# Kernel optimization log

Hardware: AMD Instinct MI355X
Metric: run time of the kernel (lower is better)

## Reference

```python
import jax, jax.numpy as jnp
import numpy as np

DIM = 512
N_HEADS = 8
HEAD_DIM = DIM // N_HEADS


def rope_pos(T, head_dim, dtype=jnp.float32):
    inv_freq = 1.0 / (10000.0 ** (jnp.arange(0, head_dim, 2, dtype=jnp.float32) / head_dim))
    t = jnp.arange(T, dtype=jnp.float32)
    freqs = jnp.einsum('i,j->ij', t, inv_freq)            # [T, head_dim/2]
    return jnp.concatenate([freqs, freqs], axis=-1).astype(dtype)  # [T, head_dim]


def rotate_half(x):
    x1, x2 = jnp.split(x, 2, axis=-1)
    return jnp.concatenate([-x2, x1], axis=-1)


def apply_rope(pos, t):
    # pos: [T, hd] -> broadcast to [1,1,T,hd]; t: [B,H,T,hd]
    pos = pos[None, None, :, :]
    return t * jnp.cos(pos) + rotate_half(t) * jnp.sin(pos)


def setup_inputs() -> dict:
    key = jax.random.key(0)
    ks = jax.random.split(key, 6)
    B, T = 4, 2048
    x = jax.random.normal(ks[0], (B, T, DIM), dtype=jnp.float32)
    mask = jnp.zeros((B, T), dtype=jnp.float32)  # additive mask
    s = 1.0 / np.sqrt(DIM)
    qkv_w = jax.random.normal(ks[1], (3 * DIM, DIM), dtype=jnp.float32) * s
    qkv_b = jnp.zeros((3 * DIM,), dtype=jnp.float32)
    proj_w = jax.random.normal(ks[2], (DIM, DIM), dtype=jnp.float32) * s
    proj_b = jnp.zeros((DIM,), dtype=jnp.float32)
    return {"x": x, "mask": mask, "qkv_w": qkv_w, "qkv_b": qkv_b,
            "proj_w": proj_w, "proj_b": proj_b}


def reference(x, mask, qkv_w, qkv_b, proj_w, proj_b):
    B, T, C = x.shape
    qkv = x @ qkv_w.T + qkv_b                       # [B,T,3C]
    qkv = qkv.reshape(B, T, 3, N_HEADS, HEAD_DIM)
    q, k, v = qkv[:, :, 0], qkv[:, :, 1], qkv[:, :, 2]  # [B,T,H,hd]
    q = q.transpose(0, 2, 1, 3)                     # [B,H,T,hd]
    k = k.transpose(0, 2, 1, 3)
    v = v.transpose(0, 2, 1, 3)
    pos = rope_pos(T, HEAD_DIM, x.dtype)
    q = apply_rope(pos, q)
    k = apply_rope(pos, k)
    scores = jnp.einsum('bhqd,bhkd->bhqk', q, k) * (1.0 / np.sqrt(HEAD_DIM))
    scores = scores + mask[:, None, None, :]        # 2D mask -> [B,1,1,T]
    probs = jax.nn.softmax(scores.astype(jnp.float32), axis=-1).astype(x.dtype)
    # dropout is identity in eval mode
    out = jnp.einsum('bhqk,bhkd->bhqd', probs, v)   # [B,H,T,hd]
    out = out.transpose(0, 2, 1, 3).reshape(B, T, C)
    return out @ proj_w.T + proj_b
```

## Files before the change

kernel.cpp:

```cpp
#include <hip/hip_runtime.h>
#include <math.h>


typedef __attribute__((ext_vector_type(8))) short bf16x8;
typedef __attribute__((ext_vector_type(4))) float floatx4;

#define LOG2E 1.44269504088896f

__device__ __forceinline__ unsigned short f2bf(float f) {
  unsigned int u = __float_as_uint(f);
  u += 0x7fffu + ((u >> 16) & 1u);
  return (unsigned short)(u >> 16);
}

__device__ __forceinline__ unsigned int cvtpk_bf16(float a, float b) {
  unsigned int r;
  asm("v_cvt_pk_bf16_f32 %0, %1, %2" : "=v"(r) : "v"(a), "v"(b));
  return r;
}

__device__ __forceinline__ void gld_lds16(unsigned short* lds, const unsigned short* g) {
  __builtin_amdgcn_global_load_lds(
      (const __attribute__((address_space(1))) unsigned int*)g,
      (__attribute__((address_space(3))) unsigned int*)lds, 16, 0, 0);
}

__global__ __launch_bounds__(256) void prep_kernel(
    const float* __restrict__ x, const float* __restrict__ wq, const float* __restrict__ wp,
    unsigned short* __restrict__ xb, unsigned short* __restrict__ wqb,
    unsigned short* __restrict__ wpb, float* __restrict__ cosT, float* __restrict__ sinT) {
  int i = blockIdx.x * 256 + threadIdx.x;
  if (i < 655360) {
    int base = i * 8;
    const float* src;
    unsigned short* dst;
    int j;
    if (base < 4194304)      { src = x;  dst = xb;  j = base; }
    else if (base < 4980736) { src = wq; dst = wqb; j = base - 4194304; }
    else                     { src = wp; dst = wpb; j = base - 4980736; }
    float4 a = *(const float4*)(src + j);
    float4 b = *(const float4*)(src + j + 4);
    uint4 r;
    r.x = cvtpk_bf16(a.x, a.y);
    r.y = cvtpk_bf16(a.z, a.w);
    r.z = cvtpk_bf16(b.x, b.y);
    r.w = cvtpk_bf16(b.z, b.w);
    *(uint4*)(dst + j) = r;
  } else if (i < 720896) {
    int j = i - 655360;
    int t = j >> 5, f = j & 31;
    double fr = (double)t * pow(10000.0, -(double)f / 32.0);
    cosT[j] = (float)cos(fr);
    sinT[j] = (float)sin(fr);
  }
}

__global__ __launch_bounds__(256) void qkv_kernel(
    const unsigned short* __restrict__ xb, const unsigned short* __restrict__ wqb,
    const float* __restrict__ qkv_b, const float* __restrict__ cosT,
    const float* __restrict__ sinT, unsigned short* __restrict__ Qb,
    unsigned short* __restrict__ Kb, unsigned short* __restrict__ Vtb) {
  __shared__ __align__(16) unsigned short SM[2][2][128 * 32];
  const int tid = threadIdx.x;
  const int wave = tid >> 6, lane = tid & 63, ln = lane & 15, quad = lane >> 4;
  const int m0 = blockIdx.x * 128, n0 = blockIdx.y * 128;
  const int wr = (wave >> 1) * 64, wc = (wave & 1) * 64;

  floatx4 acc[4][4];
#pragma unroll
  for (int i = 0; i < 4; ++i)
#pragma unroll
    for (int j = 0; j < 4; ++j) acc[i][j] = (floatx4){0.f, 0.f, 0.f, 0.f};

  const int c0 = tid, c1 = tid + 256;
  const int ar0 = c0 >> 2, ak0 = (c0 & 3) * 8;
  const int ar1 = c1 >> 2, ak1 = (c1 & 3) * 8;

  gld_lds16(SM[0][0] + c0 * 8, xb + (size_t)(m0 + ar0) * 512 + ak0);
  gld_lds16(SM[0][0] + c1 * 8, xb + (size_t)(m0 + ar1) * 512 + ak1);
  gld_lds16(SM[0][1] + c0 * 8, wqb + (size_t)(n0 + ar0) * 512 + ak0);
  gld_lds16(SM[0][1] + c1 * 8, wqb + (size_t)(n0 + ar1) * 512 + ak1);
  __syncthreads();

  for (int kt = 0; kt < 16; ++kt) {
    const int cur = kt & 1;
    if (kt < 15) {
      const int kn = (kt + 1) * 32;
      gld_lds16(SM[cur ^ 1][0] + c0 * 8, xb + (size_t)(m0 + ar0) * 512 + kn + ak0);
      gld_lds16(SM[cur ^ 1][0] + c1 * 8, xb + (size_t)(m0 + ar1) * 512 + kn + ak1);
      gld_lds16(SM[cur ^ 1][1] + c0 * 8, wqb + (size_t)(n0 + ar0) * 512 + kn + ak0);
      gld_lds16(SM[cur ^ 1][1] + c1 * 8, wqb + (size_t)(n0 + ar1) * 512 + kn + ak1);
    }
    bf16x8 af[4], bfb[4];
#pragma unroll
    for (int mi = 0; mi < 4; ++mi)
      af[mi] = *(const bf16x8*)(SM[cur][0] + (wr + mi * 16 + ln) * 32 + quad * 8);
#pragma unroll
    for (int ni = 0; ni < 4; ++ni)
      bfb[ni] = *(const bf16x8*)(SM[cur][1] + (wc + ni * 16 + ln) * 32 + quad * 8);
#pragma unroll
    for (int mi = 0; mi < 4; ++mi)
#pragma unroll
      for (int ni = 0; ni < 4; ++ni)
        acc[mi][ni] = __builtin_amdgcn_mfma_f32_16x16x32_bf16(af[mi], bfb[ni], acc[mi][ni], 0, 0, 0);
    __syncthreads();
  }

  const int colbase = n0 + wc;
  const int mat = colbase >> 9;
  float bias[4];
#pragma unroll
  for (int ni = 0; ni < 4; ++ni) bias[ni] = qkv_b[colbase + ni * 16 + ln];

  if (mat == 2) {
    unsigned short* Ts = &SM[0][0][0];
#pragma unroll
    for (int mi = 0; mi < 4; ++mi) {
      int r0 = wr + mi * 16 + quad * 4;
#pragma unroll
      for (int ni = 0; ni < 4; ++ni) {
        int c = wc + ni * 16 + ln;
        ushort4 pk;
        pk.x = f2bf(acc[mi][ni][0] + bias[ni]);
        pk.y = f2bf(acc[mi][ni][1] + bias[ni]);
        pk.z = f2bf(acc[mi][ni][2] + bias[ni]);
        pk.w = f2bf(acc[mi][ni][3] + bias[ni]);
        *(ushort4*)(Ts + c * 128 + (r0 ^ ((c & 7) << 3))) = pk;
      }
    }
    __syncthreads();
    const int d2 = tid >> 1, seg = tid & 1;
    const int h0 = (n0 & 511) >> 6;
    const int hh = d2 >> 6, dd = d2 & 63;
    const int bidx = m0 >> 11, tl0 = m0 & 2047;
    unsigned short* dst = Vtb + ((size_t)(bidx * 8 + h0 + hh) * 64 + dd) * 2048 + tl0;
    const int xr = (d2 & 7) << 3;
#pragma unroll
    for (int j = 0; j < 8; ++j) {
      int g = seg * 64 + j * 8;
      uint4 v = *(const uint4*)(Ts + d2 * 128 + (g ^ xr));
      *(uint4*)(dst + g) = v;
    }
  } else {
    const int h = (colbase & 511) >> 6;
    unsigned short* dst = (mat == 0) ? Qb : Kb;
    const float sc = (mat == 0) ? 0.125f * LOG2E : 1.0f;
#pragma unroll
    for (int mi = 0; mi < 4; ++mi) {
#pragma unroll
      for (int r = 0; r < 4; ++r) {
        int row = m0 + wr + mi * 16 + quad * 4 + r;
        int bidx = row >> 11, t = row & 2047;
        const float* cr = cosT + t * 32;
        const float* sr = sinT + t * 32;
        size_t obase = ((size_t)(bidx * 8 + h) * 2048 + t) * 64;
#pragma unroll
        for (int ni = 0; ni < 2; ++ni) {
          int dlo = ni * 16 + ln;
          float cv = cr[dlo], sv = sr[dlo];
          float xlo = acc[mi][ni][r] + bias[ni];
          float xhi = acc[mi][ni + 2][r] + bias[ni + 2];
          dst[obase + dlo]      = f2bf((xlo * cv - xhi * sv) * sc);
          dst[obase + dlo + 32] = f2bf((xhi * cv + xlo * sv) * sc);
        }
      }
    }
  }
}

__global__ __launch_bounds__(512) void attn_kernel(
    const unsigned short* __restrict__ Qb, const unsigned short* __restrict__ Kb,
    const unsigned short* __restrict__ Vtb, const float* __restrict__ mask,
    unsigned short* __restrict__ attnb) {
  __shared__ __align__(16) unsigned short Ks[2][64 * 64];
  __shared__ __align__(16) unsigned short Vs[2][64 * 64];
  __shared__ __align__(16) unsigned short Ps[128 * 64];

  const int tid = threadIdx.x;
  const int wave = tid >> 6, lane = tid & 63, ln = lane & 15, quad = lane >> 4;
  const int swz = (ln & 7) << 3;
  const int bh = blockIdx.y;
  const int b = bh >> 3, h = bh & 7;
  const int q0 = blockIdx.x * 128;
  const int wq = wave * 16;

  const unsigned short* Qhead = Qb + (size_t)bh * 2048 * 64;
  const unsigned short* Khead = Kb + (size_t)bh * 2048 * 64;
  const unsigned short* Vhead = Vtb + (size_t)bh * 64 * 2048;

  bf16x8 qf[2];
#pragma unroll
  for (int ks = 0; ks < 2; ++ks)
    qf[ks] = *(const bf16x8*)(Qhead + (size_t)(q0 + wq + ln) * 64 + ks * 32 + quad * 8);

  floatx4 o[4];
#pragma unroll
  for (int mi2 = 0; mi2 < 4; ++mi2) o[mi2] = (floatx4){0.f, 0.f, 0.f, 0.f};
  float mrun = -INFINITY;
  float lrun = 0.f;

  const int srow = tid >> 3;
  const int scol = (tid & 7) * 8;
  const int sdst = srow * 64 + (scol ^ ((srow & 7) << 3));

  {
    uint4 k0v = *(const uint4*)(Khead + (size_t)srow * 64 + scol);
    uint4 v0v = *(const uint4*)(Vhead + (size_t)srow * 2048 + scol);
    *(uint4*)(Ks[0] + sdst) = k0v;
    *(uint4*)(Vs[0] + sdst) = v0v;
  }
  __syncthreads();

  for (int kt = 0; kt < 32; ++kt) {
    const int cur = kt & 1;
    const int k0 = kt * 64;
    uint4 kpre, vpre;
    if (kt < 31) {
      kpre = *(const uint4*)(Khead + (size_t)(k0 + 64 + srow) * 64 + scol);
      vpre = *(const uint4*)(Vhead + (size_t)srow * 2048 + k0 + 64 + scol);
    }

    floatx4 sm[4];
#pragma unroll
    for (int mi = 0; mi < 4; ++mi) {
      bf16x8 kf0 = *(const bf16x8*)(Ks[cur] + (mi * 16 + ln) * 64 + ((quad * 8) ^ swz));
      bf16x8 kf1 = *(const bf16x8*)(Ks[cur] + (mi * 16 + ln) * 64 + ((32 + quad * 8) ^ swz));
      floatx4 a = (floatx4){0.f, 0.f, 0.f, 0.f};
      a = __builtin_amdgcn_mfma_f32_16x16x32_bf16(kf0, qf[0], a, 0, 0, 0);
      a = __builtin_amdgcn_mfma_f32_16x16x32_bf16(kf1, qf[1], a, 0, 0, 0);
      sm[mi] = a;
    }
#pragma unroll
    for (int mi = 0; mi < 4; ++mi) {
      float4 mv = *(const float4*)(mask + b * 2048 + k0 + mi * 16 + quad * 4);
      sm[mi][0] += mv.x * LOG2E; sm[mi][1] += mv.y * LOG2E;
      sm[mi][2] += mv.z * LOG2E; sm[mi][3] += mv.w * LOG2E;
    }
    float vmax = fmaxf(fmaxf(sm[0][0], sm[0][1]), fmaxf(sm[0][2], sm[0][3]));
#pragma unroll
    for (int mi = 1; mi < 4; ++mi)
      vmax = fmaxf(vmax, fmaxf(fmaxf(sm[mi][0], sm[mi][1]), fmaxf(sm[mi][2], sm[mi][3])));
    vmax = fmaxf(vmax, __shfl_xor(vmax, 16));
    vmax = fmaxf(vmax, __shfl_xor(vmax, 32));
    if (__any(vmax > mrun)) {
      float nm = fmaxf(mrun, vmax);
      float alpha = exp2f(mrun - nm);
      mrun = nm;
      lrun *= alpha;
#pragma unroll
      for (int mi2 = 0; mi2 < 4; ++mi2) {
        o[mi2][0] *= alpha; o[mi2][1] *= alpha;
        o[mi2][2] *= alpha; o[mi2][3] *= alpha;
      }
    }
    float psum = 0.f;
#pragma unroll
    for (int mi = 0; mi < 4; ++mi)
#pragma unroll
      for (int r = 0; r < 4; ++r) {
        float p = exp2f(sm[mi][r] - mrun);
        sm[mi][r] = p;
        psum += p;
      }
    psum += __shfl_xor(psum, 16);
    psum += __shfl_xor(psum, 32);
    lrun += psum;

#pragma unroll
    for (int mi = 0; mi < 4; ++mi) {
      uint2 pk;
      pk.x = cvtpk_bf16(sm[mi][0], sm[mi][1]);
      pk.y = cvtpk_bf16(sm[mi][2], sm[mi][3]);
      *(uint2*)(Ps + (wq + ln) * 64 + ((mi * 16 + quad * 4) ^ swz)) = pk;
    }
#pragma unroll
    for (int ks = 0; ks < 2; ++ks) {
      bf16x8 pb = *(const bf16x8*)(Ps + (wq + ln) * 64 + ((ks * 32 + quad * 8) ^ swz));
#pragma unroll
      for (int mi2 = 0; mi2 < 4; ++mi2) {
        bf16x8 vf = *(const bf16x8*)(Vs[cur] + (mi2 * 16 + ln) * 64 + ((ks * 32 + quad * 8) ^ swz));
        o[mi2] = __builtin_amdgcn_mfma_f32_16x16x32_bf16(vf, pb, o[mi2], 0, 0, 0);
      }
    }

    if (kt < 31) {
      *(uint4*)(Ks[cur ^ 1] + sdst) = kpre;
      *(uint4*)(Vs[cur ^ 1] + sdst) = vpre;
      __syncthreads();
    }
  }

  {
    float inv = 1.f / lrun;
    int t = q0 + wq + ln;
    size_t base = ((size_t)b * 2048 + t) * 512 + h * 64;
#pragma unroll
    for (int mi2 = 0; mi2 < 4; ++mi2) {
      uint2 pk;
      pk.x = cvtpk_bf16(o[mi2][0] * inv, o[mi2][1] * inv);
      pk.y = cvtpk_bf16(o[mi2][2] * inv, o[mi2][3] * inv);
      *(uint2*)(attnb + base + mi2 * 16 + quad * 4) = pk;
    }
  }
}

__global__ __launch_bounds__(512) void proj_kernel(
    const unsigned short* __restrict__ ab, const unsigned short* __restrict__ wpb,
    const float* __restrict__ proj_b, float* __restrict__ out) {
  __shared__ __align__(16) unsigned short As[2][128 * 32];
  __shared__ __align__(16) unsigned short Bs[2][128 * 32];
  const int tid = threadIdx.x;
  const int wave = tid >> 6, lane = tid & 63, ln = lane & 15, quad = lane >> 4;
  const int m0 = blockIdx.x * 128, n0 = blockIdx.y * 128;
  const int wr = (wave >> 1) * 32, wc = (wave & 1) * 64;

  floatx4 acc[2][4];
#pragma unroll
  for (int i = 0; i < 2; ++i)
#pragma unroll
    for (int j = 0; j < 4; ++j) acc[i][j] = (floatx4){0.f, 0.f, 0.f, 0.f};

  const int ar = tid >> 2, ak = (tid & 3) * 8;

  gld_lds16(As[0] + tid * 8, ab + (size_t)(m0 + ar) * 512 + ak);
  gld_lds16(Bs[0] + tid * 8, wpb + (size_t)(n0 + ar) * 512 + ak);
  __syncthreads();

  for (int kt = 0; kt < 16; ++kt) {
    const int cur = kt & 1;
    if (kt < 15) {
      const int kn = (kt + 1) * 32;
      gld_lds16(As[cur ^ 1] + tid * 8, ab + (size_t)(m0 + ar) * 512 + kn + ak);
      gld_lds16(Bs[cur ^ 1] + tid * 8, wpb + (size_t)(n0 + ar) * 512 + kn + ak);
    }
    bf16x8 af[2], bfb[4];
#pragma unroll
    for (int mi = 0; mi < 2; ++mi)
      af[mi] = *(const bf16x8*)(As[cur] + (wr + mi * 16 + ln) * 32 + quad * 8);
#pragma unroll
    for (int ni = 0; ni < 4; ++ni)
      bfb[ni] = *(const bf16x8*)(Bs[cur] + (wc + ni * 16 + ln) * 32 + quad * 8);
#pragma unroll
    for (int mi = 0; mi < 2; ++mi)
#pragma unroll
      for (int ni = 0; ni < 4; ++ni)
        acc[mi][ni] = __builtin_amdgcn_mfma_f32_16x16x32_bf16(af[mi], bfb[ni], acc[mi][ni], 0, 0, 0);
    __syncthreads();
  }

#pragma unroll
  for (int mi = 0; mi < 2; ++mi)
#pragma unroll
    for (int ni = 0; ni < 4; ++ni) {
      int col = n0 + wc + ni * 16 + ln;
      float pb = proj_b[col];
#pragma unroll
      for (int r = 0; r < 4; ++r) {
        int row = m0 + wr + mi * 16 + quad * 4 + r;
        out[(size_t)row * 512 + col] = acc[mi][ni][r] + pb;
      }
    }
}

extern "C" void kernel_launch(void* const* d_in, const int* in_sizes, int n_in,
                              void* d_out, int out_size, void* d_ws, size_t ws_size,
                              hipStream_t stream) {
  const float* x      = (const float*)d_in[0];
  const float* mask   = (const float*)d_in[1];
  const float* qkv_w  = (const float*)d_in[2];
  const float* qkv_b  = (const float*)d_in[3];
  const float* proj_w = (const float*)d_in[4];
  const float* proj_b = (const float*)d_in[5];
  float* out = (float*)d_out;

  char* ws = (char*)d_ws;
  unsigned short* xb   = (unsigned short*)(ws);
  unsigned short* wqb  = (unsigned short*)(ws + 8388608);
  unsigned short* wpb  = (unsigned short*)(ws + 9961472);
  float* cosT          = (float*)(ws + 10485760);
  float* sinT          = (float*)(ws + 10747904);
  unsigned short* Qb   = (unsigned short*)(ws + 11010048);
  unsigned short* Kb   = (unsigned short*)(ws + 19398656);
  unsigned short* Vtb  = (unsigned short*)(ws + 27787264);
  unsigned short* attnb= (unsigned short*)(ws + 36175872);

  prep_kernel<<<2816, 256, 0, stream>>>(x, qkv_w, proj_w, xb, wqb, wpb, cosT, sinT);
  dim3 g1(64, 12);
  qkv_kernel<<<g1, 256, 0, stream>>>(xb, wqb, qkv_b, cosT, sinT, Qb, Kb, Vtb);
  dim3 g2(16, 32);
  attn_kernel<<<g2, 512, 0, stream>>>(Qb, Kb, Vtb, mask, attnb);
  dim3 g3(64, 4);
  proj_kernel<<<g3, 512, 0, stream>>>(attnb, wpb, proj_b, out);
}
```

Before: 185.7 us.

## Stage Q/K epilogue through LDS, use direct global-to-LDS K/V loads, premultiply mask

The QKV epilogue now writes the rotated Q/K tiles into swizzled LDS and then stores 16-byte coalesced rows, instead of scattered 2-byte global stores. The V-transpose store is remapped so 16 threads cover each 128-element row. The attention kernel replaces register-staged K/V prefetch with global_load_lds direct copies, using a pre-swizzled source column. It also adds s_setprio around the MFMA sections and uses a tree-shaped max/sum. The mask is pre-scaled by LOG2E in the prep kernel, which adds a small extra buffer and extra work there.

```diff
diff --git a/kernel.cpp b/kernel.cpp
--- a/kernel.cpp
+++ b/kernel.cpp
@@ -6,6 +6,7 @@
 typedef __attribute__((ext_vector_type(4))) float floatx4;
 
 #define LOG2E 1.44269504088896f
+#define MAX3(a, b, c) fmaxf(fmaxf((a), (b)), (c))
 
 __device__ __forceinline__ unsigned short f2bf(float f) {
   unsigned int u = __float_as_uint(f);
@@ -27,8 +28,10 @@
 
 __global__ __launch_bounds__(256) void prep_kernel(
     const float* __restrict__ x, const float* __restrict__ wq, const float* __restrict__ wp,
+    const float* __restrict__ mask,
     unsigned short* __restrict__ xb, unsigned short* __restrict__ wqb,
-    unsigned short* __restrict__ wpb, float* __restrict__ cosT, float* __restrict__ sinT) {
+    unsigned short* __restrict__ wpb, float* __restrict__ cosT, float* __restrict__ sinT,
+    float* __restrict__ maskE) {
   int i = blockIdx.x * 256 + threadIdx.x;
   if (i < 655360) {
     int base = i * 8;
@@ -52,6 +55,14 @@
     double fr = (double)t * pow(10000.0, -(double)f / 32.0);
     cosT[j] = (float)cos(fr);
     sinT[j] = (float)sin(fr);
+  } else if (i < 721920) {
+    int j = (i - 720896) * 8;
+    float4 a = *(const float4*)(mask + j);
+    float4 b = *(const float4*)(mask + j + 4);
+    a.x *= LOG2E; a.y *= LOG2E; a.z *= LOG2E; a.w *= LOG2E;
+    b.x *= LOG2E; b.y *= LOG2E; b.z *= LOG2E; b.w *= LOG2E;
+    *(float4*)(maskE + j) = a;
+    *(float4*)(maskE + j + 4) = b;
   }
 }
 
@@ -112,8 +123,11 @@
 #pragma unroll
   for (int ni = 0; ni < 4; ++ni) bias[ni] = qkv_b[colbase + ni * 16 + ln];
 
+  unsigned short* Ls = &SM[0][0][0];
+  const int bidx = m0 >> 11, tl0 = m0 & 2047;
+  const int h0 = (n0 & 511) >> 6;
+
   if (mat == 2) {
-    unsigned short* Ts = &SM[0][0][0];
 #pragma unroll
     for (int mi = 0; mi < 4; ++mi) {
       int r0 = wr + mi * 16 + quad * 4;
@@ -125,52 +139,57 @@
         pk.y = f2bf(acc[mi][ni][1] + bias[ni]);
         pk.z = f2bf(acc[mi][ni][2] + bias[ni]);
         pk.w = f2bf(acc[mi][ni][3] + bias[ni]);
-        *(ushort4*)(Ts + c * 128 + (r0 ^ ((c & 7) << 3))) = pk;
+        *(ushort4*)(Ls + c * 128 + (r0 ^ ((c & 7) << 3))) = pk;
       }
     }
     __syncthreads();
-    const int d2 = tid >> 1, seg = tid & 1;
-    const int h0 = (n0 & 511) >> 6;
-    const int hh = d2 >> 6, dd = d2 & 63;
-    const int bidx = m0 >> 11, tl0 = m0 & 2047;
-    unsigned short* dst = Vtb + ((size_t)(bidx * 8 + h0 + hh) * 64 + dd) * 2048 + tl0;
-    const int xr = (d2 & 7) << 3;
-#pragma unroll
-    for (int j = 0; j < 8; ++j) {
-      int g = seg * 64 + j * 8;
-      uint4 v = *(const uint4*)(Ts + d2 * 128 + (g ^ xr));
-      *(uint4*)(dst + g) = v;
+    const int j2 = tid & 15, rid = tid >> 4;
+#pragma unroll
+    for (int it = 0; it < 8; ++it) {
+      int c = it * 16 + rid;
+      int hh = c >> 6, dd = c & 63;
+      uint4 v = *(const uint4*)(Ls + c * 128 + ((j2 * 8) ^ ((c & 7) << 3)));
+      *(uint4*)(Vtb + ((size_t)(bidx * 8 + h0 + hh) * 64 + dd) * 2048 + tl0 + j2 * 8) = v;
     }
   } else {
-    const int h = (colbase & 511) >> 6;
     unsigned short* dst = (mat == 0) ? Qb : Kb;
     const float sc = (mat == 0) ? 0.125f * LOG2E : 1.0f;
 #pragma unroll
     for (int mi = 0; mi < 4; ++mi) {
 #pragma unroll
       for (int r = 0; r < 4; ++r) {
-        int row = m0 + wr + mi * 16 + quad * 4 + r;
-        int bidx = row >> 11, t = row & 2047;
+        int lr = wr + mi * 16 + quad * 4 + r;
+        int t = tl0 + lr;
         const float* cr = cosT + t * 32;
         const float* sr = sinT + t * 32;
-        size_t obase = ((size_t)(bidx * 8 + h) * 2048 + t) * 64;
+        int xr = (lr & 7) << 3;
 #pragma unroll
         for (int ni = 0; ni < 2; ++ni) {
           int dlo = ni * 16 + ln;
           float cv = cr[dlo], sv = sr[dlo];
           float xlo = acc[mi][ni][r] + bias[ni];
           float xhi = acc[mi][ni + 2][r] + bias[ni + 2];
-          dst[obase + dlo]      = f2bf((xlo * cv - xhi * sv) * sc);
-          dst[obase + dlo + 32] = f2bf((xhi * cv + xlo * sv) * sc);
+          Ls[lr * 128 + ((wc + dlo) ^ xr)]      = f2bf((xlo * cv - xhi * sv) * sc);
+          Ls[lr * 128 + ((wc + dlo + 32) ^ xr)] = f2bf((xhi * cv + xlo * sv) * sc);
         }
       }
     }
+    __syncthreads();
+    const int jj = tid & 7, rowid = tid >> 3;
+#pragma unroll
+    for (int it = 0; it < 8; ++it) {
+      int hr = it * 32 + rowid;
+      int rr = hr & 127, hh = hr >> 7;
+      int c = hh * 64 + jj * 8;
+      uint4 v = *(const uint4*)(Ls + rr * 128 + (c ^ ((rr & 7) << 3)));
+      *(uint4*)(dst + ((size_t)(bidx * 8 + h0 + hh) * 2048 + tl0 + rr) * 64 + jj * 8) = v;
+    }
   }
 }
 
 __global__ __launch_bounds__(512) void attn_kernel(
     const unsigned short* __restrict__ Qb, const unsigned short* __restrict__ Kb,
-    const unsigned short* __restrict__ Vtb, const float* __restrict__ mask,
+    const unsigned short* __restrict__ Vtb, const float* __restrict__ maskE,
     unsigned short* __restrict__ attnb) {
   __shared__ __align__(16) unsigned short Ks[2][64 * 64];
   __shared__ __align__(16) unsigned short Vs[2][64 * 64];
@@ -200,27 +219,28 @@
   float lrun = 0.f;
 
   const int srow = tid >> 3;
-  const int scol = (tid & 7) * 8;
-  const int sdst = srow * 64 + (scol ^ ((srow & 7) << 3));
-
-  {
-    uint4 k0v = *(const uint4*)(Khead + (size_t)srow * 64 + scol);
-    uint4 v0v = *(const uint4*)(Vhead + (size_t)srow * 2048 + scol);
-    *(uint4*)(Ks[0] + sdst) = k0v;
-    *(uint4*)(Vs[0] + sdst) = v0v;
-  }
+  const int gcol = (((tid & 7) ^ (srow & 7)) << 3);
+  const unsigned short* ksrc = Khead + (size_t)srow * 64 + gcol;
+  const unsigned short* vsrc = Vhead + (size_t)srow * 2048 + gcol;
+  unsigned short* kdst0 = Ks[0] + tid * 8;
+  unsigned short* vdst0 = Vs[0] + tid * 8;
+  unsigned short* kdst1 = Ks[1] + tid * 8;
+  unsigned short* vdst1 = Vs[1] + tid * 8;
+
+  gld_lds16(kdst0, ksrc);
+  gld_lds16(vdst0, vsrc);
   __syncthreads();
 
   for (int kt = 0; kt < 32; ++kt) {
     const int cur = kt & 1;
     const int k0 = kt * 64;
-    uint4 kpre, vpre;
     if (kt < 31) {
-      kpre = *(const uint4*)(Khead + (size_t)(k0 + 64 + srow) * 64 + scol);
-      vpre = *(const uint4*)(Vhead + (size_t)srow * 2048 + k0 + 64 + scol);
+      gld_lds16(cur ? kdst0 : kdst1, ksrc + (size_t)(k0 + 64) * 64);
+      gld_lds16(cur ? vdst0 : vdst1, vsrc + k0 + 64);
     }
 
     floatx4 sm[4];
+    __builtin_amdgcn_s_setprio(1);
 #pragma unroll
     for (int mi = 0; mi < 4; ++mi) {
       bf16x8 kf0 = *(const bf16x8*)(Ks[cur] + (mi * 16 + ln) * 64 + ((quad * 8) ^ swz));
@@ -230,16 +250,19 @@
       a = __builtin_amdgcn_mfma_f32_16x16x32_bf16(kf1, qf[1], a, 0, 0, 0);
       sm[mi] = a;
     }
-#pragma unroll
-    for (int mi = 0; mi < 4; ++mi) {
-      float4 mv = *(const float4*)(mask + b * 2048 + k0 + mi * 16 + quad * 4);
-      sm[mi][0] += mv.x * LOG2E; sm[mi][1] += mv.y * LOG2E;
-      sm[mi][2] += mv.z * LOG2E; sm[mi][3] += mv.w * LOG2E;
-    }
-    float vmax = fmaxf(fmaxf(sm[0][0], sm[0][1]), fmaxf(sm[0][2], sm[0][3]));
-#pragma unroll
-    for (int mi = 1; mi < 4; ++mi)
-      vmax = fmaxf(vmax, fmaxf(fmaxf(sm[mi][0], sm[mi][1]), fmaxf(sm[mi][2], sm[mi][3])));
+    __builtin_amdgcn_s_setprio(0);
+#pragma unroll
+    for (int mi = 0; mi < 4; ++mi) {
+      float4 mv = *(const float4*)(maskE + b * 2048 + k0 + mi * 16 + quad * 4);
+      sm[mi][0] += mv.x; sm[mi][1] += mv.y;
+      sm[mi][2] += mv.z; sm[mi][3] += mv.w;
+    }
+    float t0 = MAX3(sm[0][0], sm[0][1], sm[0][2]);
+    float t1 = MAX3(sm[0][3], sm[1][0], sm[1][1]);
+    float t2 = MAX3(sm[1][2], sm[1][3], sm[2][0]);
+    float t3 = MAX3(sm[2][1], sm[2][2], sm[2][3]);
+    float t4 = MAX3(sm[3][0], sm[3][1], sm[3][2]);
+    float vmax = fmaxf(MAX3(t0, t1, t2), MAX3(t3, t4, sm[3][3]));
     vmax = fmaxf(vmax, __shfl_xor(vmax, 16));
     vmax = fmaxf(vmax, __shfl_xor(vmax, 32));
     if (__any(vmax > mrun)) {
@@ -253,15 +276,17 @@
         o[mi2][2] *= alpha; o[mi2][3] *= alpha;
       }
     }
-    float psum = 0.f;
-#pragma unroll
-    for (int mi = 0; mi < 4; ++mi)
-#pragma unroll
-      for (int r = 0; r < 4; ++r) {
-        float p = exp2f(sm[mi][r] - mrun);
-        sm[mi][r] = p;
-        psum += p;
-      }
+    float ps[4];
+#pragma unroll
+    for (int mi = 0; mi < 4; ++mi) {
+      float p0 = exp2f(sm[mi][0] - mrun);
+      float p1 = exp2f(sm[mi][1] - mrun);
+      float p2 = exp2f(sm[mi][2] - mrun);
+      float p3 = exp2f(sm[mi][3] - mrun);
+      sm[mi][0] = p0; sm[mi][1] = p1; sm[mi][2] = p2; sm[mi][3] = p3;
+      ps[mi] = (p0 + p1) + (p2 + p3);
+    }
+    float psum = (ps[0] + ps[1]) + (ps[2] + ps[3]);
     psum += __shfl_xor(psum, 16);
     psum += __shfl_xor(psum, 32);
     lrun += psum;
@@ -273,6 +298,7 @@
       pk.y = cvtpk_bf16(sm[mi][2], sm[mi][3]);
       *(uint2*)(Ps + (wq + ln) * 64 + ((mi * 16 + quad * 4) ^ swz)) = pk;
     }
+    __builtin_amdgcn_s_setprio(1);
 #pragma unroll
     for (int ks = 0; ks < 2; ++ks) {
       bf16x8 pb = *(const bf16x8*)(Ps + (wq + ln) * 64 + ((ks * 32 + quad * 8) ^ swz));
@@ -282,12 +308,9 @@
         o[mi2] = __builtin_amdgcn_mfma_f32_16x16x32_bf16(vf, pb, o[mi2], 0, 0, 0);
       }
     }
-
-    if (kt < 31) {
-      *(uint4*)(Ks[cur ^ 1] + sdst) = kpre;
-      *(uint4*)(Vs[cur ^ 1] + sdst) = vpre;
-      __syncthreads();
-    }
+    __builtin_amdgcn_s_setprio(0);
+
+    __syncthreads();
   }
 
   {
@@ -383,12 +406,13 @@
   unsigned short* Kb   = (unsigned short*)(ws + 19398656);
   unsigned short* Vtb  = (unsigned short*)(ws + 27787264);
   unsigned short* attnb= (unsigned short*)(ws + 36175872);
-
-  prep_kernel<<<2816, 256, 0, stream>>>(x, qkv_w, proj_w, xb, wqb, wpb, cosT, sinT);
+  float* maskE         = (float*)(ws + 44564480);
+
+  prep_kernel<<<2820, 256, 0, stream>>>(x, qkv_w, proj_w, mask, xb, wqb, wpb, cosT, sinT, maskE);
   dim3 g1(64, 12);
   qkv_kernel<<<g1, 256, 0, stream>>>(xb, wqb, qkv_b, cosT, sinT, Qb, Kb, Vtb);
   dim3 g2(16, 32);
-  attn_kernel<<<g2, 512, 0, stream>>>(Qb, Kb, Vtb, mask, attnb);
+  attn_kernel<<<g2, 512, 0, stream>>>(Qb, Kb, Vtb, maskE, attnb);
   dim3 g3(64, 4);
   proj_kernel<<<g3, 512, 0, stream>>>(attnb, wpb, proj_b, out);
 }
```

Result: no change. 187.1 us (+0.8%).
